# Performance work log

Measured on AMD Instinct MI355X. Metric: run time of the kernel, lower is better.

## Reference

```python
import jax, jax.numpy as jnp
import numpy as np

N_NODES = 50000
N_EDGES = 800000
IN_F = 256
HEADS = 8
D = 32  # out_perhead
ALPHA_SLOPE = 0.2
EPS = 1e-16


def setup_inputs() -> dict:
    key = jax.random.key(0)
    k1, k2, k3, k4, k5 = jax.random.split(key, 5)
    x = jax.random.normal(k1, (N_NODES, IN_F), dtype=jnp.float32)
    W = jax.random.normal(k2, (HEADS, IN_F, D), dtype=jnp.float32) * 0.05
    a = jax.random.normal(k3, (HEADS, 5 * D), dtype=jnp.float32) * 0.05
    src = jax.random.randint(k4, (N_EDGES,), 0, N_NODES, dtype=jnp.int32)
    dst = jax.random.randint(k5, (N_EDGES,), 0, N_NODES, dtype=jnp.int32)
    return {"x": x, "W": W, "a": a, "src": src, "dst": dst}


def reference(x, W, a, src, dst):
    n = x.shape[0]
    # per-head projection: h[n, heads, d]
    h = jnp.einsum("ni,hio->nho", x, W)
    hs = h[src]  # [E, heads, d]  (edge[0] = source)
    hd = h[dst]  # [E, heads, d]  (edge[1] = destination)
    diff = hd - hs
    # a is the concat attention vector: [src | dst | diff | abs_diff | prod]
    a1, a2, a3, a4, a5 = jnp.split(a, 5, axis=1)  # each [heads, d]
    lin = (
        jnp.einsum("ehd,hd->eh", hs, a1)
        + jnp.einsum("ehd,hd->eh", hd, a2)
        + jnp.einsum("ehd,hd->eh", diff, a3)
        + jnp.einsum("ehd,hd->eh", jnp.abs(diff), a4)
        + jnp.einsum("ehd,hd->eh", hs * hd, a5)
    )  # [E, heads]
    alpha = jnp.where(lin > 0, lin, ALPHA_SLOPE * lin)  # leaky relu
    # sparse softmax grouped by edge[0] (src)
    mx = jax.ops.segment_max(alpha, src, num_segments=n)  # [n, heads]
    e = jnp.exp(alpha - mx[src])
    s = jax.ops.segment_sum(e, src, num_segments=n)
    att = e / (s[src] + EPS)  # [E, heads]
    # spmm: out[i] = sum_{e: src_e = i} att_e * h[dst_e]
    out = jax.ops.segment_sum(att[..., None] * hd, src, num_segments=n)  # [n, heads, d]
    return out.reshape(n, HEADS * D)
```

## Files before the change

kernel.cpp:

```cpp
#include <hip/hip_runtime.h>
#include <hip/hip_bf16.h>
#include <cmath>

#define N_NODES 50000
#define N_EDGES 800000
#define NPAD 50048
#define NWORD (NPAD / 4)
#define HB 64
#define EPB 12500
#define GB 391
#define SLOT 64

typedef _Float16 h2 __attribute__((ext_vector_type(2)));
typedef _Float16 h8 __attribute__((ext_vector_type(8)));
typedef __fp16 fp16x2 __attribute__((ext_vector_type(2)));
typedef float f32x4 __attribute__((ext_vector_type(4)));

__device__ __forceinline__ h2 pkrtz(float a, float b) {
  union { fp16x2 f; h2 h; } t;
  t.f = __builtin_amdgcn_cvt_pkrtz(a, b);
  return t.h;
}

__device__ __forceinline__ float fdot2f(h2 a, h2 b, float c) {
#if __has_builtin(__builtin_amdgcn_fdot2)
  return __builtin_amdgcn_fdot2(a, b, c, false);
#else
  float d;
  asm("v_dot2_f32_f16 %0, %1, %2, %3" : "=v"(d) : "v"(a), "v"(b), "v"(c));
  return d;
#endif
}

__device__ __forceinline__ float fexp2(float x) {
#if __has_builtin(__builtin_amdgcn_exp2f)
  return __builtin_amdgcn_exp2f(x);
#else
  return exp2f(x);
#endif
}

__device__ __forceinline__ h2 habs2(h2 v) {
  union { h2 h; unsigned u; } t;
  t.h = v;
  t.u &= 0x7fff7fffu;
  return t.h;
}

template <int CTRL>
__device__ __forceinline__ float qadd(float v) {
  const int x = __builtin_amdgcn_update_dpp(0, __float_as_int(v), CTRL, 0xF, 0xF, true);
  return v + __int_as_float(x);
}
#define QX1 0xB1
#define QX2 0x4E

__global__ __launch_bounds__(512) void prep_hist(const float* __restrict__ W,
                                                 const int* __restrict__ src,
                                                 ushort* __restrict__ WTh,
                                                 unsigned* __restrict__ hist32) {
  __shared__ unsigned cnt[NWORD];
  const int b = blockIdx.x, t = threadIdx.x;
  if (b < 128) {
    const int c = b * 2 + (t >> 8), k = t & 255;
    union { _Float16 h; ushort u; } o;
    o.h = (_Float16)W[((c >> 5) * 256 + k) * 32 + (c & 31)];
    WTh[c * 256 + k] = o.u;
  } else {
    const int hb = b - 128;
    for (int i = t; i < NWORD; i += 512) cnt[i] = 0;
    __syncthreads();
    const int base = hb * EPB;
    for (int k = t; k < EPB; k += 512) {
      const int s = src[base + k];
      atomicAdd(&cnt[s >> 2], 1u << ((s & 3) * 8));
    }
    __syncthreads();
    unsigned* out = hist32 + (size_t)hb * NWORD;
    for (int i = t; i < NWORD; i += 512) out[i] = cnt[i];
  }
}

__global__ __launch_bounds__(256) void edge_offsets(unsigned* __restrict__ hist32,
                                                    unsigned* __restrict__ count32) {
  const int gid = blockIdx.x * 256 + threadIdx.x;
  if (gid >= NWORD * 4) return;
  const int nw = gid >> 2;
  const int sg = gid & 3;
  const int c0 = sg * 16;
  unsigned v[16];
#pragma unroll
  for (int j = 0; j < 16; ++j) v[j] = hist32[(size_t)(c0 + j) * NWORD + nw];
  unsigned sum = 0;
#pragma unroll
  for (int j = 0; j < 16; ++j) sum += v[j];
  const int lane = threadIdx.x & 63;
  const int qb = lane & ~3;
  const unsigned s0 = __shfl(sum, qb + 0);
  const unsigned s1 = __shfl(sum, qb + 1);
  const unsigned s2 = __shfl(sum, qb + 2);
  unsigned run = 0;
  if (sg > 0) run += s0;
  if (sg > 1) run += s1;
  if (sg > 2) run += s2;
#pragma unroll
  for (int j = 0; j < 16; ++j) {
    hist32[(size_t)(c0 + j) * NWORD + nw] = run;
    run += v[j];
  }
  if (sg == 3) count32[nw] = run;
}

__global__ __launch_bounds__(512) void scatter_gemm(
    const float* __restrict__ x, const ushort* __restrict__ WTh,
    ushort* __restrict__ hh, const int* __restrict__ src,
    const int* __restrict__ dst, const unsigned char* __restrict__ hist8,
    ushort* __restrict__ csr) {
  __shared__ __align__(16) char smem[50176];
  const int t = threadIdx.x;
  if (blockIdx.x < HB) {
    unsigned* cnt = (unsigned*)smem;
    const int hb = blockIdx.x;
    for (int i = t; i < NWORD; i += 512) cnt[i] = 0;
    __syncthreads();
    const int base = hb * EPB;
    const int4* s4p = (const int4*)(src + base);
    const int4* d4p = (const int4*)(dst + base);
    const unsigned char* off = hist8 + (size_t)hb * NPAD;
    for (int i4 = t; i4 < EPB / 4; i4 += 512) {
      const int4 s4 = s4p[i4];
      const int4 d4 = d4p[i4];
      const int ss[4] = {s4.x, s4.y, s4.z, s4.w};
      const int dd[4] = {d4.x, d4.y, d4.z, d4.w};
#pragma unroll
      for (int u = 0; u < 4; ++u) {
        const int s = ss[u];
        const int sh = (s & 3) * 8;
        const unsigned r = atomicAdd(&cnt[s >> 2], 1u << sh);
        const int rank = (r >> sh) & 0xff;
        csr[(s << 6) + off[s] + rank] = (ushort)dd[u];
      }
    }
    return;
  }
  ushort(*Xl)[130][8] = (ushort(*)[130][8])smem;
  ushort(*Wl)[256][8] = (ushort(*)[256][8])(smem + 16640);
  const int bm = (blockIdx.x - HB) * 128;
  const int w = t >> 6, lane = t & 63;
  const int wch = w >> 1, wnd = w & 1;
  const int l15 = lane & 15, l4 = lane >> 4;
  const int xr = t >> 2;
  const int q4 = t & 3;
  int xrow = bm + xr;
  xrow = xrow < N_NODES ? xrow : N_NODES - 1;
  const float* xp = x + (size_t)xrow * 256 + q4 * 16;
  f32x4 acc[4][4] = {};
  for (int ks = 0; ks < 4; ++ks) {
    const int k0 = ks * 64;
    __syncthreads();
    for (int it = w; it < 32; it += 8) {
      const int kc = it >> 2, q = it & 3;
      const int crow = q * 64 + lane;
      const ushort* gp = WTh + (size_t)crow * 256 + k0 + kc * 8;
      __builtin_amdgcn_global_load_lds(
          (const __attribute__((address_space(1))) void*)gp,
          (__attribute__((address_space(3))) void*)&Wl[kc][q * 64][0],
          16, 0, 0);
    }
    {
      const f32x4 v0 = *(const f32x4*)(xp + k0);
      const f32x4 v1 = *(const f32x4*)(xp + k0 + 4);
      const f32x4 v2 = *(const f32x4*)(xp + k0 + 8);
      const f32x4 v3 = *(const f32x4*)(xp + k0 + 12);
      union { h2 h[4]; h8 v; } u0, u1;
      u0.h[0] = pkrtz(v0[0], v0[1]); u0.h[1] = pkrtz(v0[2], v0[3]);
      u0.h[2] = pkrtz(v1[0], v1[1]); u0.h[3] = pkrtz(v1[2], v1[3]);
      u1.h[0] = pkrtz(v2[0], v2[1]); u1.h[1] = pkrtz(v2[2], v2[3]);
      u1.h[2] = pkrtz(v3[0], v3[1]); u1.h[3] = pkrtz(v3[2], v3[3]);
      *(h8*)&Xl[q4 * 2][xr][0] = u0.v;
      *(h8*)&Xl[q4 * 2 + 1][xr][0] = u1.v;
    }
    __syncthreads();
#pragma unroll
    for (int tt = 0; tt < 2; ++tt) {
      const int kc = tt * 4 + l4;
      h8 bfr[4];
#pragma unroll
      for (int j = 0; j < 4; ++j)
        bfr[j] = *(const h8*)&Xl[kc][wnd * 64 + j * 16 + l15][0];
#pragma unroll
      for (int i = 0; i < 4; ++i) {
        const h8 af = *(const h8*)&Wl[kc][wch * 64 + i * 16 + l15][0];
#pragma unroll
        for (int j = 0; j < 4; ++j)
          acc[i][j] = __builtin_amdgcn_mfma_f32_16x16x32_f16(af, bfr[j],
                                                             acc[i][j], 0, 0, 0);
      }
    }
  }
#pragma unroll
  for (int i = 0; i < 4; ++i) {
#pragma unroll
    for (int j = 0; j < 4; ++j) {
      const int node = bm + wnd * 64 + j * 16 + l15;
      if (node < N_NODES) {
        const int ch = wch * 64 + i * 16 + l4 * 4;
        union { _Float16 h[4]; ushort4 u; } o;
        o.h[0] = (_Float16)acc[i][j][0]; o.h[1] = (_Float16)acc[i][j][1];
        o.h[2] = (_Float16)acc[i][j][2]; o.h[3] = (_Float16)acc[i][j][3];
        *(ushort4*)&hh[(size_t)node * 256 + ch] = o.u;
      }
    }
  }
}

__global__ __launch_bounds__(256) void gat_edge(const ushort* __restrict__ hh,
                                                const float* __restrict__ a,
                                                const unsigned char* __restrict__ count8,
                                                const ushort* __restrict__ csr,
                                                float* __restrict__ out) {
  const int wv = threadIdx.x >> 6;
  const int lane = threadIdx.x & 63;
  const int node = blockIdx.x * 4 + wv;
  if (node >= N_NODES) return;
  const int eoff = lane >> 5;
  const int l32 = lane & 31;
  const int head = l32 >> 2;
  const int c0 = l32 * 8;
  const float* ah = a + head * 160 + ((l32 & 3) * 8);
  const float IL2 = 1.4426950408889634f;

  float a1[8], a2[8], a3[8], a4v[8], a5[8];
  *(float4*)&a1[0] = *(const float4*)(ah + 0);   *(float4*)&a1[4] = *(const float4*)(ah + 4);
  *(float4*)&a2[0] = *(const float4*)(ah + 32);  *(float4*)&a2[4] = *(const float4*)(ah + 36);
  *(float4*)&a3[0] = *(const float4*)(ah + 64);  *(float4*)&a3[4] = *(const float4*)(ah + 68);
  *(float4*)&a4v[0] = *(const float4*)(ah + 96); *(float4*)&a4v[4] = *(const float4*)(ah + 100);
  *(float4*)&a5[0] = *(const float4*)(ah + 128); *(float4*)&a5[4] = *(const float4*)(ah + 132);

  union HU { uint4 u4; h2 h[4]; };
  HU hsu;
  hsu.u4 = *(const uint4*)&hh[(size_t)node * 256 + c0];
  h2 hs2[4], b2[4], a42[4];
  float cn = 0.f;
#pragma unroll
  for (int q = 0; q < 4; ++q) {
    hs2[q] = hsu.h[q];
    const float h0 = (float)hs2[q][0], h1 = (float)hs2[q][1];
    const float b0 = (a2[2 * q] + a3[2 * q] + h0 * a5[2 * q]) * IL2;
    const float b1 = (a2[2 * q + 1] + a3[2 * q + 1] + h1 * a5[2 * q + 1]) * IL2;
    b2[q] = h2{(_Float16)b0, (_Float16)b1};
    a42[q] = h2{(_Float16)(a4v[2 * q] * IL2), (_Float16)(a4v[2 * q + 1] * IL2)};
    cn += h0 * (a1[2 * q] - a3[2 * q]) + h1 * (a1[2 * q + 1] - a3[2 * q + 1]);
  }
  cn *= IL2;
  cn = qadd<QX1>(cn);
  cn = qadd<QX2>(cn);

  float s = 0.f;
  h2 acc2[4] = {};
  const int e0 = node << 6;
  const int cnt = count8[node];
  const int e1 = e0 + cnt;

  auto PROC = [&](const HU& cur, bool cv) {
    float p1 = 0.f, p2 = 0.f;
#pragma unroll
    for (int q = 0; q < 4; ++q) {
      p1 = fdot2f(cur.h[q], b2[q], p1);
      const h2 d = cur.h[q] - hs2[q];
      p2 = fdot2f(habs2(d), a42[q], p2);
    }
    float p = p1 + p2;
    p = qadd<QX1>(p);
    p = qadd<QX2>(p);
    const float lin = cn + p;
    float alpha = fmaxf(lin, 0.2f * lin);
    alpha = cv ? alpha : -INFINITY;
    const float w = fexp2(alpha);
    s += w;
    const h2 w2 = h2{(_Float16)w, (_Float16)w};
#pragma unroll
    for (int q = 0; q < 4; ++q) acc2[q] += w2 * cur.h[q];
  };

  if (cnt > 0) {
    const int nit = (cnt + 1) >> 1;
    const int iA = e0 + eoff;
    const int iB = iA + 2;
    bool uA = iA < e1;
    bool uB = iB < e1;
    HU bufA, bufB;
    {
      const int jA = csr[iA];
      const int jB = csr[iB];
      bufA.u4 = *(const uint4*)&hh[(size_t)jA * 256 + c0];
      bufB.u4 = *(const uint4*)&hh[(size_t)jB * 256 + c0];
    }
    int nAi = iA + 4; bool vA = nAi < e1;
    int nBi = iB + 4; bool vB = nBi < e1;
    int jA2 = csr[nAi];
    int jB2 = csr[nBi];
    const int steps = (nit + 1) >> 1;
    for (int t = 0; t < steps; ++t) {
      PROC(bufA, uA);
      bufA.u4 = *(const uint4*)&hh[(size_t)jA2 * 256 + c0];
      uA = vA;
      nAi += 4; vA = nAi < e1;
      jA2 = csr[nAi];
      PROC(bufB, uB);
      bufB.u4 = *(const uint4*)&hh[(size_t)jB2 * 256 + c0];
      uB = vB;
      nBi += 4; vB = nBi < e1;
      jB2 = csr[nBi];
    }
  }
  float o[8];
#pragma unroll
  for (int q = 0; q < 4; ++q) {
    o[2 * q] = (float)acc2[q][0];
    o[2 * q + 1] = (float)acc2[q][1];
  }
  s += __shfl_xor(s, 32);
  const float inv = 1.f / (s + 1e-16f);
#pragma unroll
  for (int q = 0; q < 8; ++q) o[q] = (o[q] + __shfl_xor(o[q], 32)) * inv;
  if (eoff == 0) {
    *(float4*)&out[(size_t)node * 256 + c0] = make_float4(o[0], o[1], o[2], o[3]);
    *(float4*)&out[(size_t)node * 256 + c0 + 4] = make_float4(o[4], o[5], o[6], o[7]);
  }
}

extern "C" void kernel_launch(void* const* d_in, const int* in_sizes, int n_in,
                              void* d_out, int out_size, void* d_ws, size_t ws_size,
                              hipStream_t stream) {
  const float* x = (const float*)d_in[0];
  const float* W = (const float*)d_in[1];
  const float* a = (const float*)d_in[2];
  const int* src = (const int*)d_in[3];
  const int* dst = (const int*)d_in[4];
  float* out = (float*)d_out;

  char* ws = (char*)d_ws;
  ushort* hh = (ushort*)ws;
  size_t off = (size_t)N_NODES * 256 * 2;
  ushort* WTh = (ushort*)(ws + off);     off += 256 * 256 * 2;
  unsigned* count32 = (unsigned*)(ws + off); off += NWORD * 4;
  ushort* csr = (ushort*)(ws + off);     off += (size_t)NPAD * SLOT * 2;
  unsigned* hist32 = (unsigned*)(ws + off); off += (size_t)HB * NWORD * 4;

  prep_hist<<<128 + HB, 512, 0, stream>>>(W, src, WTh, hist32);
  edge_offsets<<<(NWORD * 4 + 255) / 256, 256, 0, stream>>>(hist32, count32);
  scatter_gemm<<<HB + GB, 512, 0, stream>>>(x, WTh, hh, src, dst,
                                            (const unsigned char*)hist32, csr);
  gat_edge<<<12500, 256, 0, stream>>>(hh, a, (const unsigned char*)count32,
                                      csr, out);
}
```

Before: 117.9 us.

## Drop edge_offsets kernel by prefix-summing histograms inside scatter, prefetch x

Result: slower. 245.1 us (+108.0%).

```diff
diff --git a/kernel.cpp b/kernel.cpp
--- a/kernel.cpp
+++ b/kernel.cpp
@@ -81,52 +81,25 @@
   }
 }
 
-__global__ __launch_bounds__(256) void edge_offsets(unsigned* __restrict__ hist32,
-                                                    unsigned* __restrict__ count32) {
-  const int gid = blockIdx.x * 256 + threadIdx.x;
-  if (gid >= NWORD * 4) return;
-  const int nw = gid >> 2;
-  const int sg = gid & 3;
-  const int c0 = sg * 16;
-  unsigned v[16];
-#pragma unroll
-  for (int j = 0; j < 16; ++j) v[j] = hist32[(size_t)(c0 + j) * NWORD + nw];
-  unsigned sum = 0;
-#pragma unroll
-  for (int j = 0; j < 16; ++j) sum += v[j];
-  const int lane = threadIdx.x & 63;
-  const int qb = lane & ~3;
-  const unsigned s0 = __shfl(sum, qb + 0);
-  const unsigned s1 = __shfl(sum, qb + 1);
-  const unsigned s2 = __shfl(sum, qb + 2);
-  unsigned run = 0;
-  if (sg > 0) run += s0;
-  if (sg > 1) run += s1;
-  if (sg > 2) run += s2;
-#pragma unroll
-  for (int j = 0; j < 16; ++j) {
-    hist32[(size_t)(c0 + j) * NWORD + nw] = run;
-    run += v[j];
-  }
-  if (sg == 3) count32[nw] = run;
-}
-
 __global__ __launch_bounds__(512) void scatter_gemm(
     const float* __restrict__ x, const ushort* __restrict__ WTh,
     ushort* __restrict__ hh, const int* __restrict__ src,
-    const int* __restrict__ dst, const unsigned char* __restrict__ hist8,
-    ushort* __restrict__ csr) {
+    const int* __restrict__ dst, const unsigned* __restrict__ hist32,
+    ushort* __restrict__ csr, unsigned* __restrict__ count32) {
   __shared__ __align__(16) char smem[50176];
   const int t = threadIdx.x;
   if (blockIdx.x < HB) {
     unsigned* cnt = (unsigned*)smem;
     const int hb = blockIdx.x;
-    for (int i = t; i < NWORD; i += 512) cnt[i] = 0;
+    for (int i = t; i < NWORD; i += 512) {
+      unsigned v = 0;
+      for (int c = 0; c < hb; ++c) v += hist32[(size_t)c * NWORD + i];
+      cnt[i] = v;
+    }
     __syncthreads();
     const int base = hb * EPB;
     const int4* s4p = (const int4*)(src + base);
     const int4* d4p = (const int4*)(dst + base);
-    const unsigned char* off = hist8 + (size_t)hb * NPAD;
     for (int i4 = t; i4 < EPB / 4; i4 += 512) {
       const int4 s4 = s4p[i4];
       const int4 d4 = d4p[i4];
@@ -138,8 +111,12 @@
         const int sh = (s & 3) * 8;
         const unsigned r = atomicAdd(&cnt[s >> 2], 1u << sh);
         const int rank = (r >> sh) & 0xff;
-        csr[(s << 6) + off[s] + rank] = (ushort)dd[u];
+        csr[(s << 6) + rank] = (ushort)dd[u];
       }
+    }
+    if (hb == HB - 1) {
+      __syncthreads();
+      for (int i = t; i < NWORD; i += 512) count32[i] = cnt[i];
     }
     return;
   }
@@ -154,10 +131,23 @@
   int xrow = bm + xr;
   xrow = xrow < N_NODES ? xrow : N_NODES - 1;
   const float* xp = x + (size_t)xrow * 256 + q4 * 16;
+  f32x4 xv0 = *(const f32x4*)(xp + 0);
+  f32x4 xv1 = *(const f32x4*)(xp + 4);
+  f32x4 xv2 = *(const f32x4*)(xp + 8);
+  f32x4 xv3 = *(const f32x4*)(xp + 12);
   f32x4 acc[4][4] = {};
   for (int ks = 0; ks < 4; ++ks) {
     const int k0 = ks * 64;
     __syncthreads();
+    {
+      union { h2 h[4]; h8 v; } u0, u1;
+      u0.h[0] = pkrtz(xv0[0], xv0[1]); u0.h[1] = pkrtz(xv0[2], xv0[3]);
+      u0.h[2] = pkrtz(xv1[0], xv1[1]); u0.h[3] = pkrtz(xv1[2], xv1[3]);
+      u1.h[0] = pkrtz(xv2[0], xv2[1]); u1.h[1] = pkrtz(xv2[2], xv2[3]);
+      u1.h[2] = pkrtz(xv3[0], xv3[1]); u1.h[3] = pkrtz(xv3[2], xv3[3]);
+      *(h8*)&Xl[q4 * 2][xr][0] = u0.v;
+      *(h8*)&Xl[q4 * 2 + 1][xr][0] = u1.v;
+    }
     for (int it = w; it < 32; it += 8) {
       const int kc = it >> 2, q = it & 3;
       const int crow = q * 64 + lane;
@@ -167,20 +157,14 @@
           (__attribute__((address_space(3))) void*)&Wl[kc][q * 64][0],
           16, 0, 0);
     }
-    {
-      const f32x4 v0 = *(const f32x4*)(xp + k0);
-      const f32x4 v1 = *(const f32x4*)(xp + k0 + 4);
-      const f32x4 v2 = *(const f32x4*)(xp + k0 + 8);
-      const f32x4 v3 = *(const f32x4*)(xp + k0 + 12);
-      union { h2 h[4]; h8 v; } u0, u1;
-      u0.h[0] = pkrtz(v0[0], v0[1]); u0.h[1] = pkrtz(v0[2], v0[3]);
-      u0.h[2] = pkrtz(v1[0], v1[1]); u0.h[3] = pkrtz(v1[2], v1[3]);
-      u1.h[0] = pkrtz(v2[0], v2[1]); u1.h[1] = pkrtz(v2[2], v2[3]);
-      u1.h[2] = pkrtz(v3[0], v3[1]); u1.h[3] = pkrtz(v3[2], v3[3]);
-      *(h8*)&Xl[q4 * 2][xr][0] = u0.v;
-      *(h8*)&Xl[q4 * 2 + 1][xr][0] = u1.v;
-    }
-    __syncthreads();
+    __syncthreads();
+    if (ks < 3) {
+      const float* p = xp + (ks + 1) * 64;
+      xv0 = *(const f32x4*)(p + 0);
+      xv1 = *(const f32x4*)(p + 4);
+      xv2 = *(const f32x4*)(p + 8);
+      xv3 = *(const f32x4*)(p + 12);
+    }
 #pragma unroll
     for (int tt = 0; tt < 2; ++tt) {
       const int kc = tt * 4 + l4;
@@ -349,9 +333,8 @@
   unsigned* hist32 = (unsigned*)(ws + off); off += (size_t)HB * NWORD * 4;
 
   prep_hist<<<128 + HB, 512, 0, stream>>>(W, src, WTh, hist32);
-  edge_offsets<<<(NWORD * 4 + 255) / 256, 256, 0, stream>>>(hist32, count32);
-  scatter_gemm<<<HB + GB, 512, 0, stream>>>(x, WTh, hh, src, dst,
-                                            (const unsigned char*)hist32, csr);
+  scatter_gemm<<<HB + GB, 512, 0, stream>>>(x, WTh, hh, src, dst, hist32,
+                                            csr, count32);
   gat_edge<<<12500, 256, 0, stream>>>(hh, a, (const unsigned char*)count32,
                                       csr, out);
 }
```
